# Optimization experiments

Hardware: AMD Instinct MI355X
Metric: run time of the kernel (lower is better)

The kernel has to match this reference:

```python
import jax, jax.numpy as jnp
import numpy as np

B, S, D, DC, H = 4, 2048, 768, 384, 12
HD = DC // H  # compressed head_dim = 32


def setup_inputs() -> dict:
    key = jax.random.key(0)
    ks = jax.random.split(key, 8)
    std = 0.02
    return {
        "hidden_states": jax.random.normal(ks[0], (B, S, D), dtype=jnp.float32),
        "W_attn": jax.random.normal(ks[1], (D, 3 * D), dtype=jnp.float32) * std,
        "b_attn": jnp.zeros((3 * D,), dtype=jnp.float32),
        "P_q": jax.random.normal(ks[2], (D, DC), dtype=jnp.float32) * std,
        "P_k": jax.random.normal(ks[3], (D, DC), dtype=jnp.float32) * std,
        "P_v": jax.random.normal(ks[4], (D, DC), dtype=jnp.float32) * std,
        "W_back": jax.random.normal(ks[5], (DC, D), dtype=jnp.float32) * std,
        "W_proj": jax.random.normal(ks[6], (D, D), dtype=jnp.float32) * std,
        "b_proj": jnp.zeros((D,), dtype=jnp.float32),
    }


def reference(hidden_states, W_attn, b_attn, P_q, P_k, P_v, W_back, W_proj, b_proj):
    b, s, _ = hidden_states.shape
    # GPT-2 Conv1D style c_attn: out = x @ W + b, then split into q,k,v
    qkv = hidden_states @ W_attn + b_attn          # [B,S,3D]
    q, k, v = jnp.split(qkv, 3, axis=-1)           # each [B,S,D]
    # sparsify hooks: per-token linear compression D -> DC
    q = q @ P_q                                    # [B,S,DC]
    k = k @ P_k
    v = v @ P_v
    # split heads -> [B,H,S,HD]
    split = lambda t: t.reshape(b, s, H, HD).transpose(0, 2, 1, 3)
    qh, kh, vh = split(q), split(k), split(v)
    # naive attention with explicit causal mask (as in original _attn)
    scores = jnp.einsum("bhqd,bhkd->bhqk", qh, kh) / jnp.sqrt(jnp.float32(HD))
    causal = jnp.tril(jnp.ones((s, s), dtype=scores.dtype))  # [S,S]
    scores = scores * causal + (-10000.0) * (1.0 - causal)
    weights = jax.nn.softmax(scores, axis=-1)
    ctx = jnp.einsum("bhqk,bhkd->bhqd", weights, vh)         # [B,H,S,HD]
    # merge heads -> [B,S,DC]
    ctx = ctx.transpose(0, 2, 1, 3).reshape(b, s, DC)
    # backproject DC -> D, then c_proj
    out = ctx @ W_back                             # [B,S,D]
    out = out @ W_proj + b_proj                    # [B,S,D]
    return out
```

## Files before the change

kernel.cpp:

```cpp
#include <hip/hip_runtime.h>
#include <math.h>


typedef unsigned short u16;
typedef unsigned int   u32;

#define VLD 8320

using short8 = __attribute__((ext_vector_type(8))) short;
using bf16x4 = __attribute__((ext_vector_type(4))) short;
using f32x4  = __attribute__((ext_vector_type(4))) float;

__device__ __forceinline__ u16 f2bf(float f) {
  u32 u = __builtin_bit_cast(u32, f);
  u = (u + 0x7fffu + ((u >> 16) & 1u)) >> 16;
  return (u16)u;
}

__device__ __forceinline__ float b2f(u16 b) {
  return __builtin_bit_cast(float, (u32)b << 16);
}

__device__ __forceinline__ u32 cvtpk_bf16(float lo, float hi) {
  u32 d;
  asm("v_cvt_pk_bf16_f32 %0, %1, %2" : "=v"(d) : "v"(lo), "v"(hi));
  return d;
}

__device__ __forceinline__ bf16x4 pack4(const f32x4 v) {
  union { u32 u[2]; bf16x4 s; } c;
  c.u[0] = cvtpk_bf16(v[0], v[1]);
  c.u[1] = cvtpk_bf16(v[2], v[3]);
  return c.s;
}

__device__ __forceinline__ float exp2v(float x) {
  return __builtin_amdgcn_exp2f(x);
}

__device__ __forceinline__ f32x4 mfma16bf(bf16x4 a, bf16x4 b, f32x4 c) {
#if __has_builtin(__builtin_amdgcn_mfma_f32_16x16x16bf16_1k)
  return __builtin_amdgcn_mfma_f32_16x16x16bf16_1k(a, b, c, 0, 0, 0);
#elif __has_builtin(__builtin_amdgcn_mfma_f32_16x16x16_bf16)
  return __builtin_amdgcn_mfma_f32_16x16x16_bf16(a, b, c, 0, 0, 0);
#else
  f32x4 d;
  asm("v_mfma_f32_16x16x16_bf16 %0, %1, %2, %3"
      : "=v"(d) : "v"(a), "v"(b), "v"(c));
  return d;
#endif
}

__device__ __forceinline__ void gload_lds16(const void* g, void* l) {
  __builtin_amdgcn_global_load_lds((__attribute__((address_space(1))) u32*)g,
                                   (__attribute__((address_space(3))) u32*)l,
                                   16, 0, 0);
}

__global__ __launch_bounds__(256) void prep_all(
    const float* __restrict__ x, const float* __restrict__ Wa,
    const float* __restrict__ Wb, const float* __restrict__ Pq,
    const float* __restrict__ Pk, const float* __restrict__ Pv,
    const float* __restrict__ Wp,
    u16* __restrict__ x_bf, u16* __restrict__ Wat_bf, u16* __restrict__ Wbk_bf,
    u16* __restrict__ PT, u16* __restrict__ WprT) {
  __shared__ float t[32][33];
  const int blk = blockIdx.x, tid = threadIdx.x;
  if (blk < 8160) {
    const float* src; u16* dst; int i;
    if (blk < 6144)      { src = x;  dst = x_bf;   i = blk * 256 + tid; }
    else if (blk < 7872) { src = Wa; dst = Wat_bf; i = (blk - 6144) * 256 + tid; }
    else                 { src = Wb; dst = Wbk_bf; i = (blk - 7872) * 256 + tid; }
    const float4 v = ((const float4*)src)[i];
    ((ushort4*)dst)[i] = make_ushort4(f2bf(v.x), f2bf(v.y), f2bf(v.z), f2bf(v.w));
    return;
  }
  const float* src; u16* dst; int C, R, bx, by;
  if (blk < 8448)      { src = Pq; dst = PT;             R = 768; C = 384; int t2 = blk - 8160; bx = t2 % 12; by = t2 / 12; }
  else if (blk < 8736) { src = Pk; dst = PT + 384 * 768; R = 768; C = 384; int t2 = blk - 8448; bx = t2 % 12; by = t2 / 12; }
  else if (blk < 9024) { src = Pv; dst = PT + 768 * 768; R = 768; C = 384; int t2 = blk - 8736; bx = t2 % 12; by = t2 / 12; }
  else                 { src = Wp; dst = WprT;           R = 768; C = 768; int t2 = blk - 9024; bx = t2 % 24; by = t2 / 24; }
  const int c0 = bx * 32, r0 = by * 32, tx = tid & 31, ty = tid >> 5;
  for (int i = ty; i < 32; i += 8)
    t[i][tx] = src[(size_t)(r0 + i) * C + c0 + tx];
  __syncthreads();
  for (int i = ty; i < 32; i += 8)
    dst[(size_t)(c0 + i) * R + r0 + tx] = f2bf(t[tx][i]);
}

template<int OBF16>
__device__ __forceinline__ void gemm_tile(
    const u16* __restrict__ A, const u16* __restrict__ BT,
    const float* __restrict__ bias, void* __restrict__ Cv,
    int K, int lda, int ldb, int ldc, int m0, int n0, int biasmode, bool slab,
    u16* As, u16* Bs) {
  const int tid = threadIdx.x;
  const int l = tid & 63, w = tid >> 6;
  const int r = l & 15, g = l >> 4;
  const int koff = slab ? (m0 / 384) * 768 : 0;
  const u16* Ap = A + ((size_t)m0 + w * 16 + r) * lda + g * 8;
  const u16* Bp = BT + ((size_t)n0 + w * 16 + r) * ldb + koff + g * 8;
  f32x4 acc[2][4] = {};
  const int wm = w >> 1, wn = w & 1;
  const int nk = K >> 5;

  auto stage = [&](int kt, int buf) {
    gload_lds16(Ap + kt,                    &As[buf * 2048 + (size_t)tid * 8]);
    gload_lds16(Bp + kt,                    &Bs[buf * 4096 + (size_t)tid * 8]);
    gload_lds16(Bp + kt + (size_t)64 * ldb, &Bs[buf * 4096 + 2048 + (size_t)tid * 8]);
  };

  stage(0, 0);
  __syncthreads();
  int cur = 0;
  for (int t = 0; t < nk; ++t) {
    if (t + 1 < nk) stage((t + 1) << 5, cur ^ 1);
    const int oa = cur * 2048, ob = cur * 4096;
    short8 af[2], bfr[4];
    #pragma unroll
    for (int i = 0; i < 2; ++i)
      af[i]  = *(const short8*)&As[oa + ((wm * 2 + i) * 64 + l) * 8];
    #pragma unroll
    for (int i = 0; i < 4; ++i)
      bfr[i] = *(const short8*)&Bs[ob + ((wn * 4 + i) * 64 + l) * 8];
    #pragma unroll
    for (int mi = 0; mi < 2; ++mi)
      #pragma unroll
      for (int ni = 0; ni < 4; ++ni)
        acc[mi][ni] = __builtin_amdgcn_mfma_f32_16x16x32_bf16(af[mi], bfr[ni],
                                                              acc[mi][ni], 0, 0, 0);
    __syncthreads();
    cur ^= 1;
  }

  const int row0 = m0 + wm * 32, col0 = n0 + wn * 64;
  #pragma unroll
  for (int ni = 0; ni < 4; ++ni) {
    const int col = col0 + ni * 16 + r;
    const float bvc = (biasmode == 1) ? bias[col] : 0.f;
    #pragma unroll
    for (int mi = 0; mi < 2; ++mi)
      #pragma unroll
      for (int j = 0; j < 4; ++j) {
        const int row = row0 + mi * 16 + 4 * g + j;
        float bv = bvc;
        if (biasmode == 2) bv = bias[row];
        const float v = acc[mi][ni][j] + bv;
        if (OBF16) ((u16*)Cv)[(size_t)row * ldc + col] = f2bf(v);
        else       ((float*)Cv)[(size_t)row * ldc + col] = v;
      }
  }
}

__global__ __launch_bounds__(256, 4) void gemm_prep(
    const u16* __restrict__ PT, const u16* __restrict__ Wat,
    const u16* __restrict__ WprT, const u16* __restrict__ Wbk,
    const float* __restrict__ ba,
    u16* __restrict__ WcT, u16* __restrict__ WbpT, float* __restrict__ bc) {
  __shared__ alignas(16) u16 As[4096], Bs[8192];
  const int t = blockIdx.x;
  if (t < 108) {
    gemm_tile<1>(PT, Wat, nullptr, WcT, 768, 768, 2304, 768,
                 (t % 18) * 64, (t / 18) * 128, 0, true, As, Bs);
  } else if (t < 144) {
    const int t2 = t - 108;
    gemm_tile<1>(WprT, Wbk, nullptr, WbpT, 768, 768, 768, 384,
                 (t2 % 12) * 64, (t2 / 12) * 128, 0, false, As, Bs);
  } else {
    const int c = (t - 144) * 144 + threadIdx.x;
    if (threadIdx.x < 144 && c < 1152) {
      const int slab = c / 384;
      const float* bs = ba + slab * 768;
      const u16* row = PT + (size_t)c * 768;
      float s = 0.f;
      for (int jj = 0; jj < 96; ++jj) {
        const short8 v = *(const short8*)&row[jj * 8];
        #pragma unroll
        for (int e = 0; e < 8; ++e)
          s = fmaf(bs[jj * 8 + e], b2f((u16)v[e]), s);
      }
      bc[c] = s;
    }
  }
}

__global__ __launch_bounds__(256, 4) void gemm_qkvt(
    const u16* __restrict__ x_bf, const u16* __restrict__ WcT,
    const float* __restrict__ bc, u16* __restrict__ QKbuf, u16* __restrict__ VTbuf) {
  __shared__ alignas(16) u16 As[4096], Bs[8192];
  const int t = blockIdx.x;
  if (t < 768) {
    gemm_tile<1>(x_bf, WcT, bc, QKbuf, 768, 768, 768, 768,
                 (t % 128) * 64, (t / 128) * 128, 1, false, As, Bs);
  } else {
    const int t2 = t - 768;
    gemm_tile<1>(WcT + (size_t)768 * 768, x_bf, bc + 768, VTbuf, 768, 768, 768, VLD,
                 (t2 % 6) * 64, (t2 / 6) * 128, 2, false, As, Bs);
  }
}

__global__ __launch_bounds__(256, 4) void gemm_out(
    const u16* __restrict__ ctx, const u16* __restrict__ WbpT,
    const float* __restrict__ bp, float* __restrict__ out) {
  __shared__ alignas(16) u16 As[4096], Bs[8192];
  const int t = blockIdx.x;
  gemm_tile<0>(ctx, WbpT, bp, out, 384, 384, 384, 768,
               (t % 128) * 64, (t / 128) * 128, 1, false, As, Bs);
}

__global__ __launch_bounds__(256, 4) void attn_kernel(
    const u16* __restrict__ QK, const u16* __restrict__ VT,
    u16* __restrict__ ctx) {
  __shared__ alignas(16) u16 Ks[2][2048];
  __shared__ alignas(16) u16 Vs[2][32 * 72];
  const int tid = threadIdx.x;
  const int w = tid >> 6, l = tid & 63;
  const int r = l & 15, g = l >> 4;
  const int idx = blockIdx.x;
  const int cc = 15 - idx / 48;
  const int bh = idx % 48;
  const int b = bh / 12, h = bh % 12;
  const size_t tok0 = (size_t)b * 2048;
  const int q0 = cc * 128 + w * 32;
  const u16* Qb = QK + (tok0 + q0) * 768 + h * 32;
  const u16* Kb = QK + tok0 * 768 + 384 + h * 32;
  const u16* Vb = VT + (size_t)(h * 32) * VLD + b * 2048;
  const float scale2 = 0.25500526474f;
  const float THR = 8.0f;
  const f32x4 fz = {0.f, 0.f, 0.f, 0.f};

  short8 qf[2];
  qf[0] = *(const short8*)&Qb[(size_t)r * 768 + 8 * g];
  qf[1] = *(const short8*)&Qb[(size_t)(16 + r) * 768 + 8 * g];

  float mrun[2] = {-3.0e38f, -3.0e38f};
  float lpart[2] = {0.f, 0.f};
  f32x4 o[2][2] = {};
  const int ntb = 2 * (cc + 1);
  const int ntw = (q0 + 31) / 64 + 1;

  const int krow = ((tid >> 6) << 4) + (tid & 15);
  const int kcol = ((tid >> 4) & 3) * 8;
  const int vd   = tid >> 3;
  const int vkc  = (tid & 7) * 8;

  uint4 vreg;
  auto stageK = [&](int t, int buf) {
    gload_lds16(&Kb[(size_t)(t * 64 + krow) * 768 + kcol], &Ks[buf][(size_t)tid * 8]);
  };
  auto loadV = [&](int t) {
    vreg = *(const uint4*)&Vb[(size_t)vd * VLD + t * 64 + vkc];
  };
  auto writeV = [&](int buf) {
    *(uint4*)&Vs[buf][vd * 72 + vkc] = vreg;
  };

  loadV(0); stageK(0, 0); writeV(0);
  __syncthreads();
  int cur = 0;
  for (int t = 0; t < ntb; ++t) {
    const bool pf = (t + 1 < ntb);
    if (pf) { loadV(t + 1); stageK(t + 1, cur ^ 1); }
    if (t < ntw) {
      short8 kf[4];
      #pragma unroll
      for (int kj = 0; kj < 4; ++kj)
        kf[kj] = *(const short8*)&Ks[cur][((kj * 64 + l)) * 8];
      bf16x4 vf[2][4];
      #pragma unroll
      for (int di = 0; di < 2; ++di)
        #pragma unroll
        for (int kj = 0; kj < 4; ++kj)
          vf[di][kj] = *(const bf16x4*)&Vs[cur][(16 * di + r) * 72 + kj * 16 + 4 * g];

      f32x4 s[2][4];
      __builtin_amdgcn_s_setprio(1);
      #pragma unroll
      for (int kj = 0; kj < 4; ++kj)
        #pragma unroll
        for (int mi = 0; mi < 2; ++mi)
          s[mi][kj] = __builtin_amdgcn_mfma_f32_16x16x32_bf16(kf[kj], qf[mi], fz, 0, 0, 0);
      __builtin_amdgcn_s_setprio(0);

      if (t == ntw - 1) {
        #pragma unroll
        for (int mi = 0; mi < 2; ++mi) {
          const int qq = q0 + mi * 16 + r;
          #pragma unroll
          for (int kj = 0; kj < 4; ++kj)
            #pragma unroll
            for (int jj = 0; jj < 4; ++jj) {
              const int kk = t * 64 + kj * 16 + 4 * g + jj;
              if (kk > qq) s[mi][kj][jj] = -3.0e38f;
            }
        }
      }

      #pragma unroll
      for (int mi = 0; mi < 2; ++mi) {
        const float a0 = fmaxf(fmaxf(s[mi][0][0], s[mi][0][1]), fmaxf(s[mi][0][2], s[mi][0][3]));
        const float a1 = fmaxf(fmaxf(s[mi][1][0], s[mi][1][1]), fmaxf(s[mi][1][2], s[mi][1][3]));
        const float a2 = fmaxf(fmaxf(s[mi][2][0], s[mi][2][1]), fmaxf(s[mi][2][2], s[mi][2][3]));
        const float a3 = fmaxf(fmaxf(s[mi][3][0], s[mi][3][1]), fmaxf(s[mi][3][2], s[mi][3][3]));
        const float lmxs = fmaxf(fmaxf(a0, a1), fmaxf(a2, a3)) * scale2;
        if (__any(lmxs > mrun[mi] + THR)) {
          float mx = lmxs;
          mx = fmaxf(mx, __shfl_xor(mx, 16));
          mx = fmaxf(mx, __shfl_xor(mx, 32));
          const float mnew = fmaxf(mrun[mi], mx);
          const float al = exp2v(mrun[mi] - mnew);
          mrun[mi] = mnew;
          lpart[mi] *= al;
          o[0][mi] *= al;
          o[1][mi] *= al;
        }
        #pragma unroll
        for (int kj = 0; kj < 4; ++kj)
          #pragma unroll
          for (int jj = 0; jj < 4; ++jj) {
            const float pv = exp2v(fmaf(s[mi][kj][jj], scale2, -mrun[mi]));
            s[mi][kj][jj] = pv;
            lpart[mi] += pv;
          }
      }

      __builtin_amdgcn_s_setprio(1);
      #pragma unroll
      for (int kj = 0; kj < 4; ++kj) {
        const bf16x4 pf0 = pack4(s[0][kj]);
        const bf16x4 pf1 = pack4(s[1][kj]);
        #pragma unroll
        for (int di = 0; di < 2; ++di) {
          o[di][0] = mfma16bf(vf[di][kj], pf0, o[di][0]);
          o[di][1] = mfma16bf(vf[di][kj], pf1, o[di][1]);
        }
      }
      __builtin_amdgcn_s_setprio(0);
    }
    if (pf) writeV(cur ^ 1);
    __syncthreads();
    cur ^= 1;
  }

  #pragma unroll
  for (int mi = 0; mi < 2; ++mi) {
    float lr = lpart[mi];
    lr += __shfl_xor(lr, 16);
    lr += __shfl_xor(lr, 32);
    const float li = 1.0f / lr;
    const size_t row = tok0 + q0 + mi * 16 + r;
    #pragma unroll
    for (int di = 0; di < 2; ++di) {
      const u32 d0 = cvtpk_bf16(o[di][mi][0] * li, o[di][mi][1] * li);
      const u32 d1 = cvtpk_bf16(o[di][mi][2] * li, o[di][mi][3] * li);
      *(uint2*)&ctx[row * 384 + h * 32 + di * 16 + 4 * g] = make_uint2(d0, d1);
    }
  }
}

extern "C" void kernel_launch(void* const* d_in, const int* in_sizes, int n_in,
                              void* d_out, int out_size, void* d_ws, size_t ws_size,
                              hipStream_t stream) {
  const float* x      = (const float*)d_in[0];
  const float* W_attn = (const float*)d_in[1];
  const float* b_attn = (const float*)d_in[2];
  const float* P_q    = (const float*)d_in[3];
  const float* P_k    = (const float*)d_in[4];
  const float* P_v    = (const float*)d_in[5];
  const float* W_back = (const float*)d_in[6];
  const float* W_proj = (const float*)d_in[7];
  const float* b_proj = (const float*)d_in[8];

  char* ws = (char*)d_ws;
  u16*   x_bf   = (u16*)(ws);
  u16*   ctx    = (u16*)(ws);
  u16*   Wat_bf = (u16*)(ws + 12582912);
  u16*   PT     = (u16*)(ws + 16121856);
  u16*   Wbk_bf = (u16*)(ws + 17891328);
  u16*   WprT   = (u16*)(ws + 18481152);
  u16*   WcT    = (u16*)(ws + 19660800);
  u16*   WbpT   = (u16*)(ws + 21430272);
  float* bc     = (float*)(ws + 22020096);
  u16*   QKbuf  = (u16*)d_out;
  u16*   VTbuf  = (u16*)((char*)d_out + 12582912);
  float* out    = (float*)d_out;

  prep_all<<<9600, 256, 0, stream>>>(x, W_attn, W_back, P_q, P_k, P_v, W_proj,
                                     x_bf, Wat_bf, Wbk_bf, PT, WprT);
  gemm_prep<<<152, 256, 0, stream>>>(PT, Wat_bf, WprT, Wbk_bf, b_attn, WcT, WbpT, bc);
  gemm_qkvt<<<1152, 256, 0, stream>>>(x_bf, WcT, bc, QKbuf, VTbuf);
  attn_kernel<<<768, 256, 0, stream>>>(QKbuf, VTbuf, ctx);
  gemm_out<<<768, 256, 0, stream>>>(ctx, WbpT, b_proj, out);
}
```

Before: 132.6 us.

## Deepen GEMM LDS pipeline with manual waitcnt and remap tiles for XCD locality

Rewrites the GEMM tile main loop to keep two stages of global-to-LDS loads in flight, using explicit vmcnt waits, raw ds_read_b128 through precomputed LDS addresses, and a barrier placed after the fragment reads so the next stage can be issued before the MFMAs. It also remaps block indices in both GEMM kernels so that blocks landing on the same XCD (index modulo 8) work on neighbouring tiles sharing A/B rows. The goal is to hide global load latency and improve L2 reuse. Hand-written waitcnt counts depend on exactly three loads per stage and are fragile if that changes.

Result: faster. 129.5 us (-2.3%).

```diff
diff --git a/kernel.cpp b/kernel.cpp
--- a/kernel.cpp
+++ b/kernel.cpp
@@ -55,6 +55,10 @@
   __builtin_amdgcn_global_load_lds((__attribute__((address_space(1))) u32*)g,
                                    (__attribute__((address_space(3))) u32*)l,
                                    16, 0, 0);
+}
+
+__device__ __forceinline__ u32 lds_u32(const void* p) {
+  return (u32)(size_t)(const __attribute__((address_space(3))) char*)p;
 }
 
 __global__ __launch_bounds__(256) void prep_all(
@@ -104,6 +108,9 @@
   const int wm = w >> 1, wn = w & 1;
   const int nk = K >> 5;
 
+  const u32 abase = lds_u32(As) + (u32)(wm * 2048 + l * 16);
+  const u32 bbase = lds_u32(Bs) + (u32)(wn * 4096 + l * 16);
+
   auto stage = [&](int kt, int buf) {
     gload_lds16(Ap + kt,                    &As[buf * 2048 + (size_t)tid * 8]);
     gload_lds16(Bp + kt,                    &Bs[buf * 4096 + (size_t)tid * 8]);
@@ -111,25 +118,33 @@
   };
 
   stage(0, 0);
-  __syncthreads();
+  stage(32, 1);
   int cur = 0;
   for (int t = 0; t < nk; ++t) {
-    if (t + 1 < nk) stage((t + 1) << 5, cur ^ 1);
-    const int oa = cur * 2048, ob = cur * 4096;
+    if (t + 1 < nk) asm volatile("s_waitcnt vmcnt(3)" ::: "memory");
+    else            asm volatile("s_waitcnt vmcnt(0)" ::: "memory");
+    __builtin_amdgcn_s_barrier();
+    __builtin_amdgcn_sched_barrier(0);
+    const u32 aoff = (u32)cur << 12;
+    const u32 boff = (u32)cur << 13;
     short8 af[2], bfr[4];
     #pragma unroll
     for (int i = 0; i < 2; ++i)
-      af[i]  = *(const short8*)&As[oa + ((wm * 2 + i) * 64 + l) * 8];
+      asm volatile("ds_read_b128 %0, %1" : "=v"(af[i])  : "v"(abase + aoff + 1024u * i));
     #pragma unroll
     for (int i = 0; i < 4; ++i)
-      bfr[i] = *(const short8*)&Bs[ob + ((wn * 4 + i) * 64 + l) * 8];
+      asm volatile("ds_read_b128 %0, %1" : "=v"(bfr[i]) : "v"(bbase + boff + 1024u * i));
+    asm volatile("s_waitcnt lgkmcnt(0)" ::: "memory");
+    __builtin_amdgcn_sched_barrier(0);
+    __builtin_amdgcn_s_barrier();
+    __builtin_amdgcn_sched_barrier(0);
+    if (t + 2 < nk) stage((t + 2) << 5, cur);
     #pragma unroll
     for (int mi = 0; mi < 2; ++mi)
       #pragma unroll
       for (int ni = 0; ni < 4; ++ni)
         acc[mi][ni] = __builtin_amdgcn_mfma_f32_16x16x32_bf16(af[mi], bfr[ni],
                                                               acc[mi][ni], 0, 0, 0);
-    __syncthreads();
     cur ^= 1;
   }
 
@@ -189,13 +204,15 @@
     const float* __restrict__ bc, u16* __restrict__ QKbuf, u16* __restrict__ VTbuf) {
   __shared__ alignas(16) u16 As[4096], Bs[8192];
   const int t = blockIdx.x;
-  if (t < 768) {
+  const int w = (t & 7) * 144 + (t >> 3);
+  const int sid = w / 18, j = w % 18;
+  if (j < 12) {
     gemm_tile<1>(x_bf, WcT, bc, QKbuf, 768, 768, 768, 768,
-                 (t % 128) * 64, (t / 128) * 128, 1, false, As, Bs);
+                 sid * 128 + (j & 1) * 64, (j >> 1) * 128, 1, false, As, Bs);
   } else {
-    const int t2 = t - 768;
+    const int j2 = j - 12;
     gemm_tile<1>(WcT + (size_t)768 * 768, x_bf, bc + 768, VTbuf, 768, 768, 768, VLD,
-                 (t2 % 6) * 64, (t2 / 6) * 128, 2, false, As, Bs);
+                 j2 * 64, sid * 128, 2, false, As, Bs);
   }
 }
 
@@ -204,8 +221,9 @@
     const float* __restrict__ bp, float* __restrict__ out) {
   __shared__ alignas(16) u16 As[4096], Bs[8192];
   const int t = blockIdx.x;
+  const int w = (t & 7) * 96 + (t >> 3);
   gemm_tile<0>(ctx, WbpT, bp, out, 384, 384, 384, 768,
-               (t % 128) * 64, (t / 128) * 128, 1, false, As, Bs);
+               (w / 6) * 64, (w % 6) * 128, 1, false, As, Bs);
 }
 
 __global__ __launch_bounds__(256, 4) void attn_kernel(
```
